# Kernel optimization log

Hardware: AMD Instinct MI355X
Metric: run time of the kernel (lower is better)

## Reference

```python
import jax, jax.numpy as jnp
import numpy as np

INV_SQRT2 = 0.7071067811865476  # Haar/db1 filter coefficient
LEVEL = 3


def _split(x, axis):
    """One Haar analysis step along `axis` (even length assumed)."""
    ax = axis % x.ndim
    sl0 = [slice(None)] * x.ndim; sl0[ax] = slice(0, None, 2)
    sl1 = [slice(None)] * x.ndim; sl1[ax] = slice(1, None, 2)
    x0, x1 = x[tuple(sl0)], x[tuple(sl1)]
    return (x0 + x1) * INV_SQRT2, (x0 - x1) * INV_SQRT2


def _merge(lo, hi, axis):
    """One Haar synthesis step along `axis` (interleave even/odd)."""
    ax = axis % lo.ndim
    e = (lo + hi) * INV_SQRT2
    o = (lo - hi) * INV_SQRT2
    s = jnp.stack([e, o], axis=ax + 1)
    shape = list(lo.shape)
    shape[ax] *= 2
    return s.reshape(shape)


def _dwt2(x):
    lo, hi = _split(x, -1)
    a, h = _split(lo, -2)
    v, d = _split(hi, -2)
    return a, h, v, d


def _idwt2(a, h, v, d):
    lo = _merge(a, h, -2)
    hi = _merge(v, d, -2)
    return _merge(lo, hi, -1)


def setup_inputs() -> dict:
    key = jax.random.key(0)
    ks = jax.random.split(key, 8)
    B, H, W = 16, 1024, 1024
    x = jax.random.normal(ks[0], (B, H, W, 1), dtype=jnp.float32)
    na = (H // 8) * (W // 8)   # approx size at level 3
    n2 = (H // 4) * (W // 4)
    n1 = (H // 2) * (W // 2)
    scale = 0.02
    Wa = jax.random.normal(ks[1], (na, 1), dtype=jnp.float32) * scale
    ba = jnp.zeros((1,), jnp.float32)
    Wd1 = jax.random.normal(ks[2], (3 * na, 3), dtype=jnp.float32) * scale  # coarsest details
    bd1 = jnp.zeros((3,), jnp.float32)
    Wd2 = jax.random.normal(ks[3], (3 * n2, 3), dtype=jnp.float32) * scale
    bd2 = jnp.zeros((3,), jnp.float32)
    Wd3 = jax.random.normal(ks[4], (3 * n1, 3), dtype=jnp.float32) * scale  # finest details
    bd3 = jnp.zeros((3,), jnp.float32)
    return {"x": x, "Wa": Wa, "ba": ba, "Wd1": Wd1, "bd1": bd1,
            "Wd2": Wd2, "bd2": bd2, "Wd3": Wd3, "bd3": bd3}


def reference(x, Wa, ba, Wd1, bd1, Wd2, bd2, Wd3, bd3):
    img = x[..., 0]                      # [B, H, W]
    B = img.shape[0]
    details = []                         # finest -> coarsest
    cur = img
    for _ in range(LEVEL):
        cur, h, v, d = _dwt2(cur)
        details.append((h, v, d))
    # approximation attention: sigmoid(Dense(1)) scalar gate per sample
    aw = jax.nn.sigmoid(cur.reshape(B, -1) @ Wa + ba)   # [B, 1]
    rec = cur * aw[:, :, None]                           # [B, H/8, W/8]
    # detail attention per level (coarsest first, matching pywt coeff order)
    det_params = [(Wd1, bd1), (Wd2, bd2), (Wd3, bd3)]
    for (h, v, d), (Wd, bd) in zip(reversed(details), det_params):
        flat = jnp.stack([h, v, d], axis=1).reshape(B, -1)      # [B, 3*hl*wl]
        w = jax.nn.softmax(flat @ Wd + bd, axis=-1)             # [B, 3]
        rec = _idwt2(rec,
                     h * w[:, 0, None, None],
                     v * w[:, 1, None, None],
                     d * w[:, 2, None, None])
    return rec                                                   # [B, H, W]
```

## Files before the change

### kernel.cpp

```cpp
#include <hip/hip_runtime.h>
#include <math.h>

#define HH 1024
#define WW 1024
#define N1 262144
#define N2 65536
#define N3 16384

#define C_INV_SQRT2 0.70710678118654752440f

static __device__ __forceinline__ void haar_fwd(float P, float Q, float R, float S,
                                                float& a, float& h, float& v, float& d) {
    const float C = C_INV_SQRT2;
    float lo0 = (P + Q) * C, lo1 = (R + S) * C;
    float hi0 = (P - Q) * C, hi1 = (R - S) * C;
    a = (lo0 + lo1) * C; h = (lo0 - lo1) * C;
    v = (hi0 + hi1) * C; d = (hi0 - hi1) * C;
}

static __device__ __forceinline__ void haar_inv(float a, float h, float v, float d,
                                                float& P, float& Q, float& R, float& S) {
    const float C = C_INV_SQRT2;
    float elo = (a + h) * C, olo = (a - h) * C;
    float ehi = (v + d) * C, ohi = (v - d) * C;
    P = (elo + ehi) * C; Q = (elo - ehi) * C;
    R = (olo + ohi) * C; S = (olo - ohi) * C;
}

__global__ __launch_bounds__(256) void wa_fwd_dots(
    const float* __restrict__ x,
    const float* __restrict__ Wa,
    const float* __restrict__ Wd1,
    const float* __restrict__ Wd2,
    const float* __restrict__ Wd3,
    float* __restrict__ logits)
{
    const int b = blockIdx.z;
    const int t = threadIdx.x;
    const int tr = t >> 4, tc = t & 15;
    const int y0 = blockIdx.y * 128 + tr * 8;
    const int x0 = blockIdx.x * 128 + tc * 8;

    const float* xb = x + (size_t)b * HH * WW;

    float p[8][8];
    #pragma unroll
    for (int r = 0; r < 8; ++r) {
        const float4* row = (const float4*)(xb + (size_t)(y0 + r) * WW + x0);
        float4 u0 = row[0], u1 = row[1];
        p[r][0] = u0.x; p[r][1] = u0.y; p[r][2] = u0.z; p[r][3] = u0.w;
        p[r][4] = u1.x; p[r][5] = u1.y; p[r][6] = u1.z; p[r][7] = u1.w;
    }

    float acc[10];
    #pragma unroll
    for (int k = 0; k < 10; ++k) acc[k] = 0.f;

    float a1[4][4];
    #pragma unroll
    for (int i = 0; i < 4; ++i) {
        #pragma unroll
        for (int j = 0; j < 4; ++j) {
            float a, h, v, d;
            haar_fwd(p[2*i][2*j], p[2*i][2*j+1], p[2*i+1][2*j], p[2*i+1][2*j+1], a, h, v, d);
            a1[i][j] = a;
            size_t jj = (size_t)((y0 >> 1) + i) * 512 + (size_t)((x0 >> 1) + j);
            const float* wh = Wd3 + jj * 3;
            const float* wv = Wd3 + (jj + (size_t)N1) * 3;
            const float* wd = Wd3 + (jj + (size_t)2 * N1) * 3;
            #pragma unroll
            for (int c = 0; c < 3; ++c)
                acc[7 + c] += h * wh[c] + v * wv[c] + d * wd[c];
        }
    }

    float a2[2][2];
    #pragma unroll
    for (int i = 0; i < 2; ++i) {
        #pragma unroll
        for (int j = 0; j < 2; ++j) {
            float a, h, v, d;
            haar_fwd(a1[2*i][2*j], a1[2*i][2*j+1], a1[2*i+1][2*j], a1[2*i+1][2*j+1], a, h, v, d);
            a2[i][j] = a;
            size_t jj = (size_t)((y0 >> 2) + i) * 256 + (size_t)((x0 >> 2) + j);
            const float* wh = Wd2 + jj * 3;
            const float* wv = Wd2 + (jj + (size_t)N2) * 3;
            const float* wd = Wd2 + (jj + (size_t)2 * N2) * 3;
            #pragma unroll
            for (int c = 0; c < 3; ++c)
                acc[4 + c] += h * wh[c] + v * wv[c] + d * wd[c];
        }
    }

    {
        float a, h, v, d;
        haar_fwd(a2[0][0], a2[0][1], a2[1][0], a2[1][1], a, h, v, d);
        size_t jj = (size_t)(y0 >> 3) * 128 + (size_t)(x0 >> 3);
        acc[0] += a * Wa[jj];
        const float* wh = Wd1 + jj * 3;
        const float* wv = Wd1 + (jj + (size_t)N3) * 3;
        const float* wd = Wd1 + (jj + (size_t)2 * N3) * 3;
        #pragma unroll
        for (int c = 0; c < 3; ++c)
            acc[1 + c] += h * wh[c] + v * wv[c] + d * wd[c];
    }

    #pragma unroll
    for (int k = 0; k < 10; ++k) {
        float s = acc[k];
        #pragma unroll
        for (int off = 32; off > 0; off >>= 1) s += __shfl_down(s, off, 64);
        acc[k] = s;
    }
    __shared__ float red[4][10];
    const int lane = t & 63, wave = t >> 6;
    if (lane == 0) {
        #pragma unroll
        for (int k = 0; k < 10; ++k) red[wave][k] = acc[k];
    }
    __syncthreads();
    if (t < 10) {
        float s = red[0][t] + red[1][t] + red[2][t] + red[3][t];
        atomicAdd(&logits[b * 10 + t], s);
    }
}

__global__ void wa_gates(const float* __restrict__ logits,
                         const float* __restrict__ ba,
                         const float* __restrict__ bd1,
                         const float* __restrict__ bd2,
                         const float* __restrict__ bd3,
                         float* __restrict__ gates, int B)
{
    int t = threadIdx.x;
    if (t >= B) return;
    const float* L = logits + t * 10;
    float* G = gates + t * 10;
    G[0] = 1.f / (1.f + expf(-(L[0] + ba[0])));
    const float* bds[3] = { bd1, bd2, bd3 };
    for (int lv = 0; lv < 3; ++lv) {
        float l0 = L[1 + 3*lv + 0] + bds[lv][0];
        float l1 = L[1 + 3*lv + 1] + bds[lv][1];
        float l2 = L[1 + 3*lv + 2] + bds[lv][2];
        float m = fmaxf(l0, fmaxf(l1, l2));
        float e0 = expf(l0 - m), e1 = expf(l1 - m), e2 = expf(l2 - m);
        float inv = 1.f / (e0 + e1 + e2);
        G[1 + 3*lv + 0] = e0 * inv;
        G[1 + 3*lv + 1] = e1 * inv;
        G[1 + 3*lv + 2] = e2 * inv;
    }
}

__global__ __launch_bounds__(256) void wa_recon(
    const float* __restrict__ x,
    const float* __restrict__ gates,
    float* __restrict__ out)
{
    const int b = blockIdx.z;
    __shared__ float g[10];
    if (threadIdx.x < 10) g[threadIdx.x] = gates[b * 10 + threadIdx.x];
    __syncthreads();

    const int t = threadIdx.x;
    const int tr = t >> 4, tc = t & 15;
    const int y0 = blockIdx.y * 128 + tr * 8;
    const int x0 = blockIdx.x * 128 + tc * 8;

    const float* xb = x + (size_t)b * HH * WW;

    float p[8][8];
    #pragma unroll
    for (int r = 0; r < 8; ++r) {
        const float4* row = (const float4*)(xb + (size_t)(y0 + r) * WW + x0);
        float4 u0 = row[0], u1 = row[1];
        p[r][0] = u0.x; p[r][1] = u0.y; p[r][2] = u0.z; p[r][3] = u0.w;
        p[r][4] = u1.x; p[r][5] = u1.y; p[r][6] = u1.z; p[r][7] = u1.w;
    }

    float a1[4][4], h1[4][4], v1[4][4], d1[4][4];
    #pragma unroll
    for (int i = 0; i < 4; ++i)
        #pragma unroll
        for (int j = 0; j < 4; ++j)
            haar_fwd(p[2*i][2*j], p[2*i][2*j+1], p[2*i+1][2*j], p[2*i+1][2*j+1],
                     a1[i][j], h1[i][j], v1[i][j], d1[i][j]);

    float a2[2][2], h2[2][2], v2[2][2], d2[2][2];
    #pragma unroll
    for (int i = 0; i < 2; ++i)
        #pragma unroll
        for (int j = 0; j < 2; ++j)
            haar_fwd(a1[2*i][2*j], a1[2*i][2*j+1], a1[2*i+1][2*j], a1[2*i+1][2*j+1],
                     a2[i][j], h2[i][j], v2[i][j], d2[i][j]);

    float a3, h3, v3, d3;
    haar_fwd(a2[0][0], a2[0][1], a2[1][0], a2[1][1], a3, h3, v3, d3);

    a3 *= g[0];
    float r2[2][2];
    haar_inv(a3, h3 * g[1], v3 * g[2], d3 * g[3],
             r2[0][0], r2[0][1], r2[1][0], r2[1][1]);

    float r1[4][4];
    #pragma unroll
    for (int i = 0; i < 2; ++i)
        #pragma unroll
        for (int j = 0; j < 2; ++j)
            haar_inv(r2[i][j], h2[i][j] * g[4], v2[i][j] * g[5], d2[i][j] * g[6],
                     r1[2*i][2*j], r1[2*i][2*j+1], r1[2*i+1][2*j], r1[2*i+1][2*j+1]);

    float r0[8][8];
    #pragma unroll
    for (int i = 0; i < 4; ++i)
        #pragma unroll
        for (int j = 0; j < 4; ++j)
            haar_inv(r1[i][j], h1[i][j] * g[7], v1[i][j] * g[8], d1[i][j] * g[9],
                     r0[2*i][2*j], r0[2*i][2*j+1], r0[2*i+1][2*j], r0[2*i+1][2*j+1]);

    float* ob = out + (size_t)b * HH * WW;
    #pragma unroll
    for (int r = 0; r < 8; ++r) {
        float4* row = (float4*)(ob + (size_t)(y0 + r) * WW + x0);
        float4 u0, u1;
        u0.x = r0[r][0]; u0.y = r0[r][1]; u0.z = r0[r][2]; u0.w = r0[r][3];
        u1.x = r0[r][4]; u1.y = r0[r][5]; u1.z = r0[r][6]; u1.w = r0[r][7];
        row[0] = u0; row[1] = u1;
    }
}

extern "C" void kernel_launch(void* const* d_in, const int* in_sizes, int n_in,
                              void* d_out, int out_size, void* d_ws, size_t ws_size,
                              hipStream_t stream) {
    const float* x   = (const float*)d_in[0];
    const float* Wa  = (const float*)d_in[1];
    const float* ba  = (const float*)d_in[2];
    const float* Wd1 = (const float*)d_in[3];
    const float* bd1 = (const float*)d_in[4];
    const float* Wd2 = (const float*)d_in[5];
    const float* bd2 = (const float*)d_in[6];
    const float* Wd3 = (const float*)d_in[7];
    const float* bd3 = (const float*)d_in[8];
    float* out = (float*)d_out;

    const int B = in_sizes[0] / (HH * WW);

    float* logits = (float*)d_ws;
    float* gates  = logits + B * 10;

    hipMemsetAsync(logits, 0, (size_t)B * 10 * sizeof(float), stream);

    dim3 grid(WW / 128, HH / 128, B);
    wa_fwd_dots<<<grid, 256, 0, stream>>>(x, Wa, Wd1, Wd2, Wd3, logits);
    wa_gates<<<1, 64, 0, stream>>>(logits, ba, bd1, bd2, bd3, gates, B);
    wa_recon<<<grid, 256, 0, stream>>>(x, gates, out);
}
```

Baseline: 173.7 us.

## Fuse gate computation into recon, vectorize weight loads, use single-wave blocks

```diff
diff --git a/kernel.cpp b/kernel.cpp
--- a/kernel.cpp
+++ b/kernel.cpp
@@ -27,7 +27,7 @@
     R = (olo + ohi) * C; S = (olo - ohi) * C;
 }
 
-__global__ __launch_bounds__(256) void wa_fwd_dots(
+__global__ __launch_bounds__(64) void wa_fwd_dots(
     const float* __restrict__ x,
     const float* __restrict__ Wa,
     const float* __restrict__ Wd1,
@@ -37,9 +37,9 @@
 {
     const int b = blockIdx.z;
     const int t = threadIdx.x;
-    const int tr = t >> 4, tc = t & 15;
-    const int y0 = blockIdx.y * 128 + tr * 8;
-    const int x0 = blockIdx.x * 128 + tc * 8;
+    const int tr = t >> 3, tc = t & 7;
+    const int y0 = blockIdx.y * 64 + tr * 8;
+    const int x0 = blockIdx.x * 64 + tc * 8;
 
     const float* xb = x + (size_t)b * HH * WW;
 
@@ -59,43 +59,61 @@
     float a1[4][4];
     #pragma unroll
     for (int i = 0; i < 4; ++i) {
+        const size_t jj0 = (size_t)((y0 >> 1) + i) * 512 + (size_t)(x0 >> 1);
+        float wh[12], wv[12], wd[12];
+        {
+            const float4* H = (const float4*)(Wd3 + jj0 * 3);
+            const float4* V = (const float4*)(Wd3 + (jj0 + (size_t)N1) * 3);
+            const float4* D = (const float4*)(Wd3 + (jj0 + (size_t)2 * N1) * 3);
+            #pragma unroll
+            for (int q = 0; q < 3; ++q) {
+                float4 a = H[q]; wh[4*q] = a.x; wh[4*q+1] = a.y; wh[4*q+2] = a.z; wh[4*q+3] = a.w;
+                float4 c = V[q]; wv[4*q] = c.x; wv[4*q+1] = c.y; wv[4*q+2] = c.z; wv[4*q+3] = c.w;
+                float4 e = D[q]; wd[4*q] = e.x; wd[4*q+1] = e.y; wd[4*q+2] = e.z; wd[4*q+3] = e.w;
+            }
+        }
         #pragma unroll
         for (int j = 0; j < 4; ++j) {
             float a, h, v, d;
             haar_fwd(p[2*i][2*j], p[2*i][2*j+1], p[2*i+1][2*j], p[2*i+1][2*j+1], a, h, v, d);
             a1[i][j] = a;
-            size_t jj = (size_t)((y0 >> 1) + i) * 512 + (size_t)((x0 >> 1) + j);
-            const float* wh = Wd3 + jj * 3;
-            const float* wv = Wd3 + (jj + (size_t)N1) * 3;
-            const float* wd = Wd3 + (jj + (size_t)2 * N1) * 3;
             #pragma unroll
             for (int c = 0; c < 3; ++c)
-                acc[7 + c] += h * wh[c] + v * wv[c] + d * wd[c];
+                acc[7 + c] += h * wh[j*3 + c] + v * wv[j*3 + c] + d * wd[j*3 + c];
         }
     }
 
     float a2[2][2];
     #pragma unroll
     for (int i = 0; i < 2; ++i) {
+        const size_t jj0 = (size_t)((y0 >> 2) + i) * 256 + (size_t)(x0 >> 2);
+        float wh[6], wv[6], wd[6];
+        {
+            const float2* H = (const float2*)(Wd2 + jj0 * 3);
+            const float2* V = (const float2*)(Wd2 + (jj0 + (size_t)N2) * 3);
+            const float2* D = (const float2*)(Wd2 + (jj0 + (size_t)2 * N2) * 3);
+            #pragma unroll
+            for (int q = 0; q < 3; ++q) {
+                float2 a = H[q]; wh[2*q] = a.x; wh[2*q+1] = a.y;
+                float2 c = V[q]; wv[2*q] = c.x; wv[2*q+1] = c.y;
+                float2 e = D[q]; wd[2*q] = e.x; wd[2*q+1] = e.y;
+            }
+        }
         #pragma unroll
         for (int j = 0; j < 2; ++j) {
             float a, h, v, d;
             haar_fwd(a1[2*i][2*j], a1[2*i][2*j+1], a1[2*i+1][2*j], a1[2*i+1][2*j+1], a, h, v, d);
             a2[i][j] = a;
-            size_t jj = (size_t)((y0 >> 2) + i) * 256 + (size_t)((x0 >> 2) + j);
-            const float* wh = Wd2 + jj * 3;
-            const float* wv = Wd2 + (jj + (size_t)N2) * 3;
-            const float* wd = Wd2 + (jj + (size_t)2 * N2) * 3;
             #pragma unroll
             for (int c = 0; c < 3; ++c)
-                acc[4 + c] += h * wh[c] + v * wv[c] + d * wd[c];
+                acc[4 + c] += h * wh[j*3 + c] + v * wv[j*3 + c] + d * wd[j*3 + c];
         }
     }
 
     {
         float a, h, v, d;
         haar_fwd(a2[0][0], a2[0][1], a2[1][0], a2[1][1], a, h, v, d);
-        size_t jj = (size_t)(y0 >> 3) * 128 + (size_t)(x0 >> 3);
+        const size_t jj = (size_t)(y0 >> 3) * 128 + (size_t)(x0 >> 3);
         acc[0] += a * Wa[jj];
         const float* wh = Wd1 + jj * 3;
         const float* wv = Wd1 + (jj + (size_t)N3) * 3;
@@ -112,59 +130,50 @@
         for (int off = 32; off > 0; off >>= 1) s += __shfl_down(s, off, 64);
         acc[k] = s;
     }
-    __shared__ float red[4][10];
-    const int lane = t & 63, wave = t >> 6;
-    if (lane == 0) {
-        #pragma unroll
-        for (int k = 0; k < 10; ++k) red[wave][k] = acc[k];
-    }
-    __syncthreads();
-    if (t < 10) {
-        float s = red[0][t] + red[1][t] + red[2][t] + red[3][t];
-        atomicAdd(&logits[b * 10 + t], s);
-    }
-}
-
-__global__ void wa_gates(const float* __restrict__ logits,
-                         const float* __restrict__ ba,
-                         const float* __restrict__ bd1,
-                         const float* __restrict__ bd2,
-                         const float* __restrict__ bd3,
-                         float* __restrict__ gates, int B)
-{
-    int t = threadIdx.x;
-    if (t >= B) return;
-    const float* L = logits + t * 10;
-    float* G = gates + t * 10;
-    G[0] = 1.f / (1.f + expf(-(L[0] + ba[0])));
-    const float* bds[3] = { bd1, bd2, bd3 };
-    for (int lv = 0; lv < 3; ++lv) {
-        float l0 = L[1 + 3*lv + 0] + bds[lv][0];
-        float l1 = L[1 + 3*lv + 1] + bds[lv][1];
-        float l2 = L[1 + 3*lv + 2] + bds[lv][2];
-        float m = fmaxf(l0, fmaxf(l1, l2));
-        float e0 = expf(l0 - m), e1 = expf(l1 - m), e2 = expf(l2 - m);
-        float inv = 1.f / (e0 + e1 + e2);
-        G[1 + 3*lv + 0] = e0 * inv;
-        G[1 + 3*lv + 1] = e1 * inv;
-        G[1 + 3*lv + 2] = e2 * inv;
-    }
-}
-
-__global__ __launch_bounds__(256) void wa_recon(
+    if (t == 0) {
+        #pragma unroll
+        for (int k = 0; k < 10; ++k)
+            atomicAdd(&logits[b * 10 + k], acc[k]);
+    }
+}
+
+__global__ __launch_bounds__(64) void wa_recon(
     const float* __restrict__ x,
-    const float* __restrict__ gates,
+    const float* __restrict__ logits,
+    const float* __restrict__ ba,
+    const float* __restrict__ bd1,
+    const float* __restrict__ bd2,
+    const float* __restrict__ bd3,
     float* __restrict__ out)
 {
     const int b = blockIdx.z;
+    const int t = threadIdx.x;
+
     __shared__ float g[10];
-    if (threadIdx.x < 10) g[threadIdx.x] = gates[b * 10 + threadIdx.x];
+    if (t < 10) {
+        const float* L = logits + b * 10;
+        float val;
+        if (t == 0) {
+            val = 1.f / (1.f + expf(-(L[0] + ba[0])));
+        } else {
+            const int grp = (t - 1) / 3;
+            const int idx = (t - 1) - grp * 3;
+            const float* bd = (grp == 0) ? bd1 : (grp == 1) ? bd2 : bd3;
+            const float l0 = L[1 + 3*grp + 0] + bd[0];
+            const float l1 = L[1 + 3*grp + 1] + bd[1];
+            const float l2 = L[1 + 3*grp + 2] + bd[2];
+            const float m  = fmaxf(l0, fmaxf(l1, l2));
+            const float e0 = expf(l0 - m), e1 = expf(l1 - m), e2 = expf(l2 - m);
+            const float li = (idx == 0) ? l0 : (idx == 1) ? l1 : l2;
+            val = expf(li - m) / (e0 + e1 + e2);
+        }
+        g[t] = val;
+    }
     __syncthreads();
 
-    const int t = threadIdx.x;
-    const int tr = t >> 4, tc = t & 15;
-    const int y0 = blockIdx.y * 128 + tr * 8;
-    const int x0 = blockIdx.x * 128 + tc * 8;
+    const int tr = t >> 3, tc = t & 7;
+    const int y0 = blockIdx.y * 64 + tr * 8;
+    const int x0 = blockIdx.x * 64 + tc * 8;
 
     const float* xb = x + (size_t)b * HH * WW;
 
@@ -245,12 +254,9 @@
     const int B = in_sizes[0] / (HH * WW);
 
     float* logits = (float*)d_ws;
-    float* gates  = logits + B * 10;
-
     hipMemsetAsync(logits, 0, (size_t)B * 10 * sizeof(float), stream);
 
-    dim3 grid(WW / 128, HH / 128, B);
-    wa_fwd_dots<<<grid, 256, 0, stream>>>(x, Wa, Wd1, Wd2, Wd3, logits);
-    wa_gates<<<1, 64, 0, stream>>>(logits, ba, bd1, bd2, bd3, gates, B);
-    wa_recon<<<grid, 256, 0, stream>>>(x, gates, out);
-}
+    dim3 grid(WW / 64, HH / 64, B);
+    wa_fwd_dots<<<grid, 64, 0, stream>>>(x, Wa, Wd1, Wd2, Wd3, logits);
+    wa_recon<<<grid, 64, 0, stream>>>(x, logits, ba, bd1, bd2, bd3, out);
+}
```

Result: slower. 289.7 us (+66.8%).
